# Optimization experiments

Hardware: AMD Instinct MI355X
Metric: run time of the kernel (lower is better)

## Reference

```python
import jax, jax.numpy as jnp
import numpy as np

B, P, E, A, M, D, V, L = 32, 196, 256, 512, 512, 512, 20000, 52


def setup_inputs() -> dict:
    key = jax.random.key(0)
    ks = jax.random.split(key, 16)
    u = lambda k, sh, s=0.05: (jax.random.normal(k, sh, jnp.float32) * s)
    lengths = jnp.sort(jax.random.randint(ks[2], (B,), 2, L + 1))[::-1].at[0].set(L)
    return dict(
        encoder_out=jax.random.normal(ks[0], (B, P, E), jnp.float32),
        encoded_captions=jax.random.randint(ks[1], (B, L), 0, V),
        caption_lengths=lengths,
        W_enc_att=u(ks[3], (E, A)), b_enc_att=jnp.zeros((A,), jnp.float32),
        W_dec_att=u(ks[4], (D, A)), b_dec_att=jnp.zeros((A,), jnp.float32),
        W_full_att=u(ks[5], (A, 1)), b_full_att=jnp.zeros((1,), jnp.float32),
        emb=u(ks[6], (V, M), 0.1),
        W_ih=u(ks[7], (M + E, 4 * D)), b_ih=jnp.zeros((4 * D,), jnp.float32),
        W_hh=u(ks[8], (D, 4 * D)), b_hh=jnp.zeros((4 * D,), jnp.float32),
        W_init_h=u(ks[9], (E, D)), b_init_h=jnp.zeros((D,), jnp.float32),
        W_init_c=u(ks[10], (E, D)), b_init_c=jnp.zeros((D,), jnp.float32),
        W_fbeta=u(ks[11], (D, E)), b_fbeta=jnp.zeros((E,), jnp.float32),
        W_fc=u(ks[12], (D, V), 0.1), b_fc=jnp.zeros((V,), jnp.float32),
    )


def reference(encoder_out, encoded_captions, caption_lengths,
              W_enc_att, b_enc_att, W_dec_att, b_dec_att, W_full_att, b_full_att,
              emb, W_ih, b_ih, W_hh, b_hh,
              W_init_h, b_init_h, W_init_c, b_init_c,
              W_fbeta, b_fbeta, W_fc, b_fc):
    # Dropout is identity in eval mode.
    T = encoded_captions.shape[1] - 1  # max decode length (max caption_length - 1)
    decode_lengths = caption_lengths - 1
    embs = emb[encoded_captions]                       # [B, L, M]
    mean_enc = encoder_out.mean(axis=1)                # [B, E]
    h0 = mean_enc @ W_init_h + b_init_h                # [B, D]
    c0 = mean_enc @ W_init_c + b_init_c
    att1 = encoder_out @ W_enc_att + b_enc_att         # [B, P, A], constant over time
    masks = (jnp.arange(T)[None, :] < decode_lengths[:, None]).T  # [T, B]
    emb_seq = jnp.swapaxes(embs[:, :T, :], 0, 1)       # [T, B, M]

    def step(carry, xs):
        h, c = carry
        e_t, m = xs                                    # [B, M], [B]
        att2 = h @ W_dec_att + b_dec_att               # [B, A]
        att = (jax.nn.relu(att1 + att2[:, None, :]) @ W_full_att)[..., 0] + b_full_att[0]  # [B, P]
        alpha = jax.nn.softmax(att, axis=1)            # [B, P]
        awe = jnp.einsum('bpe,bp->be', encoder_out, alpha)
        gate = jax.nn.sigmoid(h @ W_fbeta + b_fbeta)
        awe = gate * awe
        gates = jnp.concatenate([e_t, awe], axis=1) @ W_ih + b_ih + h @ W_hh + b_hh
        i, f, g, o = jnp.split(gates, 4, axis=1)       # torch LSTMCell gate order: i, f, g, o
        c_new = jax.nn.sigmoid(f) * c + jax.nn.sigmoid(i) * jnp.tanh(g)
        h_new = jax.nn.sigmoid(o) * jnp.tanh(c_new)
        preds = h_new @ W_fc + b_fc                    # [B, V]
        mm = m[:, None]
        # rows with l <= t are frozen (they were sliced away in the torch loop)
        h = jnp.where(mm, h_new, h)
        c = jnp.where(mm, c_new, c)
        preds = jnp.where(mm, preds, 0.0)
        alpha = jnp.where(mm, alpha, 0.0)
        return (h, c), (preds, alpha)

    (_, _), (preds, alphas) = jax.lax.scan(step, (h0, c0), (emb_seq, masks))
    predictions = jnp.swapaxes(preds, 0, 1)            # [B, T, V]
    alphas = jnp.swapaxes(alphas, 0, 1)                # [B, T, P]
    return predictions, encoded_captions, decode_lengths, alphas
```

## Files before the change

kernel.cpp:

```cpp
#include <hip/hip_runtime.h>
#include <hip/hip_bf16.h>
#include <math.h>
#include <stddef.h>


typedef unsigned short ushort_t;
typedef __bf16 bf16x8 __attribute__((ext_vector_type(8)));
typedef float f32x4 __attribute__((ext_vector_type(4)));
typedef unsigned short ushort8 __attribute__((ext_vector_type(8)));
typedef unsigned short ushort4v __attribute__((ext_vector_type(4)));
typedef unsigned long long u64_t;

union FragU { ushort8 u; bf16x8 b; };

__device__ __forceinline__ unsigned short f2bu(float f){
  union { float f; unsigned int i; } c; c.f = f;
  unsigned int x = c.i;
  unsigned int r = x + 0x7fffu + ((x >> 16) & 1u);
  return (unsigned short)(r >> 16);
}
__device__ __forceinline__ float bu2f(unsigned short u){
  union { unsigned int i; float f; } c; c.i = ((unsigned int)u) << 16; return c.f;
}
__device__ __forceinline__ float sigm(float x){ return 1.f/(1.f+__expf(-x)); }
__device__ __forceinline__ float ftanh(float x){ float e = __expf(2.f*x); return 1.f - 2.f/(e+1.f); }

__device__ __forceinline__ u64_t coh_ld64(const u64_t* p){
  return __hip_atomic_load(p, __ATOMIC_RELAXED, __HIP_MEMORY_SCOPE_AGENT);
}
__device__ __forceinline__ void coh_st64(u64_t* p, u64_t v){
  __hip_atomic_store(p, v, __ATOMIC_RELAXED, __HIP_MEMORY_SCOPE_AGENT);
}
__device__ __forceinline__ int coh_ldi(const int* p){
  return __hip_atomic_load(p, __ATOMIC_RELAXED, __HIP_MEMORY_SCOPE_AGENT);
}
__device__ __forceinline__ void coh_sti(int* p, int v){
  __hip_atomic_store(p, v, __ATOMIC_RELAXED, __HIP_MEMORY_SCOPE_AGENT);
}

#define FLG(f) ((f)*32)

__global__ __launch_bounds__(256) void k_cvtT(const float* __restrict__ src, int C,
                                              ushort_t* __restrict__ dst, int ldd, int perm){
  __shared__ float tile[32][33];
  int c0 = blockIdx.x*32, r0 = blockIdx.y*32;
  int tx = threadIdx.x & 31, ty = threadIdx.x >> 5;
  #pragma unroll
  for (int i=0;i<4;i++){ int r = ty + i*8; tile[r][tx] = src[(size_t)(r0+r)*C + c0+tx]; }
  __syncthreads();
  #pragma unroll
  for (int i=0;i<4;i++){
    int c = ty + i*8;
    int row = c0 + c;
    if (perm) row = ((row & 511) << 2) | (row >> 9);
    dst[(size_t)row*ldd + r0+tx] = f2bu(tile[tx][c]);
  }
}

__global__ __launch_bounds__(256) void k_cvt4(const float* __restrict__ src,
                                              ushort_t* __restrict__ dst, int n4){
  int i = blockIdx.x*256 + threadIdx.x;
  if (i < n4){
    float4 v = ((const float4*)src)[i];
    ushort4v o; o.x=f2bu(v.x); o.y=f2bu(v.y); o.z=f2bu(v.z); o.w=f2bu(v.w);
    ((ushort4v*)dst)[i] = o;
  }
}

__global__ __launch_bounds__(256) void k_misc(const int* __restrict__ cap, const int* __restrict__ lens,
                      const float* __restrict__ bdec, const float* __restrict__ bfb,
                      const float* __restrict__ bih, const float* __restrict__ bhh,
                      float* out_cap, float* out_dl, int* declen,
                      float* xbias, float* bihR, int* flags){
  int tid = blockIdx.x*256 + threadIdx.x;
  for (int i=tid; i<5120; i+=2048) flags[i] = 0;
  if (tid < 32*52) out_cap[tid] = (float)cap[tid];
  if (tid < 32){ int dl = lens[tid]-1; out_dl[tid] = (float)dl; declen[tid] = dl; }
  if (tid < 768) xbias[tid] = (tid<512) ? bdec[tid] : bfb[tid-512];
  if (tid < 2048){
    int c = (tid&3)*512 + (tid>>2);
    bihR[tid] = bih[c] + bhh[c];
  }
}

__global__ __launch_bounds__(256) void k_init(const float* __restrict__ enc,
                     const float* __restrict__ Wih_, const float* __restrict__ bih_,
                     const float* __restrict__ Wic_, const float* __restrict__ bic_,
                     ushort_t* __restrict__ hnewb, float* __restrict__ cbuf){
  int b = blockIdx.x, tid = threadIdx.x;
  __shared__ float mean_s[256];
  const float* eb = enc + (size_t)b*196*256;
  float s = 0.f;
  for (int p=0;p<196;p++) s += eb[p*256 + tid];
  mean_s[tid] = s * (1.f/196.f);
  __syncthreads();
  float h0=0.f,h1=0.f,c0=0.f,c1=0.f;
  for (int k=0;k<256;k++){
    float m = mean_s[k];
    h0 += m*Wih_[k*512+tid];      h1 += m*Wih_[k*512+tid+256];
    c0 += m*Wic_[k*512+tid];      c1 += m*Wic_[k*512+tid+256];
  }
  hnewb[b*512+tid]     = f2bu(h0 + bih_[tid]);
  hnewb[b*512+tid+256] = f2bu(h1 + bih_[tid+256]);
  cbuf[b*512+tid]      = c0 + bic_[tid];
  cbuf[b*512+tid+256]  = c1 + bic_[tid+256];
}

__global__ __launch_bounds__(256) void k_gather(const int* __restrict__ cap,
                                                const float* __restrict__ emb,
                                                ushort_t* __restrict__ erowsb){
  int row = blockIdx.x; int b = row/51, t = row%51;
  int tok = cap[b*52 + t];
  const float* src = emb + (size_t)tok*512;
  ushort_t* dst = erowsb + (size_t)row*512;
  dst[threadIdx.x]       = f2bu(src[threadIdx.x]);
  dst[threadIdx.x + 256] = f2bu(src[threadIdx.x + 256]);
}

#define LDT 40
__global__ __launch_bounds__(256)
void k_gemm(const ushort_t* __restrict__ Ag, int lda,
            const ushort_t* __restrict__ Bg, int ldb,
            int Mrows, int Ncols, int K,
            const float* __restrict__ bias,
            float* __restrict__ outF, ushort_t* __restrict__ outH, int ldo)
{
  __shared__ ushort_t As[128*LDT];
  __shared__ ushort_t Bs[128*LDT];
  int m0 = blockIdx.y*128, n0 = blockIdx.x*128;
  int tid = threadIdx.x;
  int wave = tid>>6, lane = tid&63;
  int wm = wave>>1, wn = wave&1;
  int q = lane>>4, r = lane&15;
  f32x4 acc[4][4];
  f32x4 zero4 = {0.f,0.f,0.f,0.f};
  #pragma unroll
  for(int i=0;i<4;i++){ acc[i][0]=zero4; acc[i][1]=zero4; acc[i][2]=zero4; acc[i][3]=zero4; }

  for (int k0=0; k0<K; k0+=32){
    __syncthreads();
    #pragma unroll
    for (int c=tid; c<512; c+=256){
      int row = c>>2, ko = (c&3)*8;
      ushort8 v = {0,0,0,0,0,0,0,0};
      if (m0+row < Mrows) v = *(const ushort8*)(Ag + (size_t)(m0+row)*lda + k0 + ko);
      *(ushort8*)(As + row*LDT + ko) = v;
      ushort8 wv = {0,0,0,0,0,0,0,0};
      if (n0+row < Ncols) wv = *(const ushort8*)(Bg + (size_t)(n0+row)*ldb + k0 + ko);
      *(ushort8*)(Bs + row*LDT + ko) = wv;
    }
    __syncthreads();
    FragU a[4], bb[4];
    #pragma unroll
    for(int i=0;i<4;i++){
      a[i].u  = *(const ushort8*)(As + (64*wm + 16*i + r)*LDT + 8*q);
      bb[i].u = *(const ushort8*)(Bs + (64*wn + 16*i + r)*LDT + 8*q);
    }
    #pragma unroll
    for(int i=0;i<4;i++)
      #pragma unroll
      for(int j=0;j<4;j++)
        acc[i][j] = __builtin_amdgcn_mfma_f32_16x16x32_bf16(a[i].b, bb[j].b, acc[i][j], 0,0,0);
  }
  #pragma unroll
  for(int i=0;i<4;i++){
    int rowbase = m0 + 64*wm + 16*i + q*4;
    #pragma unroll
    for(int j=0;j<4;j++){
      int col = n0 + 64*wn + 16*j + r;
      if (col >= Ncols) continue;
      float bv = bias ? bias[col] : 0.f;
      #pragma unroll
      for(int rr=0;rr<4;rr++){
        int row = rowbase + rr;
        if (row >= Mrows) continue;
        float v = acc[i][j][rr] + bv;
        if (outF) outF[(size_t)row*ldo + col] = v;
        else      outH[(size_t)row*ldo + col] = f2bu(v);
      }
    }
  }
}

__global__ __launch_bounds__(512)
void k_steps(const ushort_t* __restrict__ XWT768, const ushort_t* __restrict__ WHCp,
             const float* __restrict__ xbias,
             const ushort_t* __restrict__ att1b, const float* __restrict__ wfull,
             const ushort_t* __restrict__ encb, const ushort_t* __restrict__ eihR,
             const int* __restrict__ declen,
             ushort_t* __restrict__ hnewb, float* __restrict__ cbuf,
             float* __restrict__ XO,
             ushort_t* __restrict__ xaweb, ushort_t* __restrict__ hallb,
             float* __restrict__ out_alph,
             const ushort_t* __restrict__ WfcT, const float* __restrict__ bfc,
             float* __restrict__ out_preds, int* flags)
{
  __shared__ char pool[150272];
  int blk = blockIdx.x, tid = threadIdx.x;
  int wave = tid>>6, lane = tid&63;
  int q = lane>>4, r = lane&15;

  if (blk < 32){
    int b = blk, g = b>>4;
    float*    att2_s = (float*)pool;
    float*    wf_s   = (float*)(pool + 3072);
    float*    part_s = (float*)(pool + 5120);
    float*    awep_s = (float*)(pool + 6848);
    float*    alpha_s= (float*)(pool + 8896);
    float*    red_s  = (float*)(pool + 9728);
    ushort_t* xst    = (ushort_t*)(pool + 9856);
    if (tid < 512) wf_s[tid] = wfull[tid];
    __syncthreads();

    for (int t=0;t<51;t++){
      if (tid < 32) while (coh_ldi(flags + FLG(g*32 + tid)) < t+1) __builtin_amdgcn_s_sleep(1);
      __syncthreads();
      {
        const u64_t* src = (const u64_t*)(XO + (size_t)b*768);
        if (tid < 384) ((u64_t*)att2_s)[tid] = coh_ld64(src + tid);
      }
      __syncthreads();
      {
        int ph = tid>>8, p = tid&255;
        if (p < 196){
          const ushort_t* arow = att1b + ((size_t)b*196 + p)*512 + ph*256;
          const float* a2 = att2_s + ph*256;
          const float* wf = wf_s + ph*256;
          float s0=0.f,s1=0.f,s2=0.f,s3=0.f;
          for (int k=0;k<256;k+=8){
            ushort8 v = *(const ushort8*)(arow + k);
            s0 += fmaxf(bu2f(v[0]) + a2[k+0], 0.f)*wf[k+0];
            s1 += fmaxf(bu2f(v[1]) + a2[k+1], 0.f)*wf[k+1];
            s2 += fmaxf(bu2f(v[2]) + a2[k+2], 0.f)*wf[k+2];
            s3 += fmaxf(bu2f(v[3]) + a2[k+3], 0.f)*wf[k+3];
            s0 += fmaxf(bu2f(v[4]) + a2[k+4], 0.f)*wf[k+4];
            s1 += fmaxf(bu2f(v[5]) + a2[k+5], 0.f)*wf[k+5];
            s2 += fmaxf(bu2f(v[6]) + a2[k+6], 0.f)*wf[k+6];
            s3 += fmaxf(bu2f(v[7]) + a2[k+7], 0.f)*wf[k+7];
          }
          part_s[ph*208 + p] = (s0+s1)+(s2+s3);
        }
      }
      __syncthreads();
      float av = -1e30f;
      if (tid < 196) av = part_s[tid] + part_s[208 + tid];
      float m = av;
      #pragma unroll
      for (int off=32;off>0;off>>=1) m = fmaxf(m, __shfl_down(m, off, 64));
      if ((tid&63)==0) red_s[tid>>6] = m;
      __syncthreads();
      if (tid==0){
        float mm = red_s[0];
        #pragma unroll
        for (int i=1;i<8;i++) mm = fmaxf(mm, red_s[i]);
        red_s[16] = mm;
      }
      __syncthreads();
      float gmax = red_s[16];
      float ev = (tid<196) ? __expf(av - gmax) : 0.f;
      float ssum = ev;
      #pragma unroll
      for (int off=32;off>0;off>>=1) ssum += __shfl_down(ssum, off, 64);
      if ((tid&63)==0) red_s[20+(tid>>6)] = ssum;
      __syncthreads();
      if (tid==0){
        float s = 0.f;
        #pragma unroll
        for (int i=0;i<8;i++) s += red_s[20+i];
        red_s[17] = s;
      }
      __syncthreads();
      float inv = 1.f/red_s[17];
      int mask = (t < declen[b]) ? 1 : 0;
      if (tid<196){
        float al = ev*inv;
        alpha_s[tid] = al;
        out_alph[((size_t)b*51 + t)*196 + tid] = mask ? al : 0.f;
      }
      __syncthreads();
      {
        int e = tid&255, hh = tid>>8;
        const ushort_t* eb = encb + (size_t)b*196*256;
        float a0=0.f, a1=0.f;
        for (int pp=0;pp<98;pp+=2){
          int p0 = hh*98 + pp;
          a0 += alpha_s[p0]  *bu2f(eb[(size_t)p0*256 + e]);
          a1 += alpha_s[p0+1]*bu2f(eb[(size_t)(p0+1)*256 + e]);
        }
        awep_s[hh*256 + e] = a0+a1;
      }
      __syncthreads();
      if (tid < 256){
        float aw = awep_s[tid] + awep_s[256+tid];
        float gate = sigm(att2_s[512 + tid]);
        xst[tid] = f2bu(gate*aw);
      }
      __syncthreads();
      if (tid < 64){
        u64_t v = *(const u64_t*)(xst + tid*4);
        coh_st64((u64_t*)(xaweb + (size_t)b*256) + tid, v);
      }
      __syncthreads();
      if (tid==0) coh_sti(flags + FLG(128 + b), t+1);
    }
  } else if (blk < 96){
    int j = blk-32, g = j>>5, jj = j&31;
    int b0 = g*16;
    int n0b = jj*64;
    int n0x = jj*32;
    ushort_t* Wh = (ushort_t*)pool;
    ushort_t* Wc = (ushort_t*)(pool + 66560);
    ushort_t* Wx = (ushort_t*)(pool + 100352);
    ushort_t* As = (ushort_t*)(pool + 133632);
    float*    gl = (float*)(pool + 142080);
    ushort_t* hst= (ushort_t*)(pool + 146176);
    ushort_t* hstA=(ushort_t*)(pool + 146688);

    for (int i=tid; i<64*64; i+=512){ int row=i>>6, ko=(i&63)*8;
      *(ushort8*)(Wh + row*520 + ko) = *(const ushort8*)(WHCp + (size_t)(n0b+row)*768 + ko); }
    for (int i=tid; i<64*32; i+=512){ int row=i>>5, ko=(i&31)*8;
      *(ushort8*)(Wc + row*264 + ko) = *(const ushort8*)(WHCp + (size_t)(n0b+row)*768 + 512 + ko); }
    if (jj < 24)
      for (int i=tid; i<32*64; i+=512){ int row=i>>6, ko=(i&63)*8;
        *(ushort8*)(Wx + row*520 + ko) = *(const ushort8*)(XWT768 + (size_t)(n0x+row)*512 + ko); }
    __syncthreads();

    f32x4 gwh = {0.f,0.f,0.f,0.f};
    float hprev = 0.f;
    {
      const u64_t* H8 = (const u64_t*)(hnewb + (size_t)b0*512);
      for (int i=tid; i<2048; i+=512){ int row=i>>7, k4=i&127;
        *(u64_t*)(As + row*520 + k4*4) = coh_ld64(H8 + row*128 + k4); }
      __syncthreads();
      if (tid < 256) hprev = bu2f(As[(tid>>4)*520 + jj*16 + (tid&15)]);
      if (jj>=24 && tid==0) coh_sti(flags + FLG(g*32+jj), 1);
      if (jj<24 && wave<2){
        f32x4 xo = {0.f,0.f,0.f,0.f};
        for (int kc=0;kc<512;kc+=32){
          FragU a,bx;
          a.u  = *(const ushort8*)(As + r*520 + kc + 8*q);
          bx.u = *(const ushort8*)(Wx + (wave*16 + r)*520 + kc + 8*q);
          xo = __builtin_amdgcn_mfma_f32_16x16x32_bf16(bx.b, a.b, xo, 0,0,0);
        }
        int col0 = n0x + wave*16 + 4*q;
        float vv[4];
        #pragma unroll
        for (int rr=0;rr<4;rr++) vv[rr] = xo[rr] + xbias[col0+rr];
        u64_t* dst = (u64_t*)(XO + (size_t)(b0 + r)*768 + col0);
        coh_st64(dst+0, ((const u64_t*)vv)[0]);
        coh_st64(dst+1, ((const u64_t*)vv)[1]);
      }
      __syncthreads();
      if (jj<24 && tid==0) coh_sti(flags + FLG(g*32+jj), 1);
      if (wave < 4){
        for (int kc=0;kc<512;kc+=32){
          FragU a,bw;
          a.u  = *(const ushort8*)(As + r*520 + kc + 8*q);
          bw.u = *(const ushort8*)(Wh + (wave*16 + r)*520 + kc + 8*q);
          gwh = __builtin_amdgcn_mfma_f32_16x16x32_bf16(a.b, bw.b, gwh, 0,0,0);
        }
      }
    }

    for (int t=0;t<51;t++){
      float eih[4] = {0.f,0.f,0.f,0.f};
      if (wave < 4){
        #pragma unroll
        for (int rr=0;rr<4;rr++){
          int row = 4*q + rr;
          eih[rr] = bu2f(eihR[((size_t)(b0+row)*51 + t)*2048 + n0b + wave*16 + r]);
        }
      }
      if (tid < 16) while (coh_ldi(flags + FLG(128 + b0 + tid)) < t+1) __builtin_amdgcn_s_sleep(1);
      __syncthreads();
      const u64_t* X8 = (const u64_t*)(xaweb + (size_t)b0*256);
      for (int i=tid; i<1024; i+=512){ int row=i>>6, k4=i&63;
        *(u64_t*)(As + row*264 + k4*4) = coh_ld64(X8 + row*64 + k4); }
      __syncthreads();
      if (wave < 4){
        f32x4 cc = {0.f,0.f,0.f,0.f};
        for (int kc=0;kc<256;kc+=32){
          FragU a,bw;
          a.u  = *(const ushort8*)(As + r*264 + kc + 8*q);
          bw.u = *(const ushort8*)(Wc + (wave*16 + r)*264 + kc + 8*q);
          cc = __builtin_amdgcn_mfma_f32_16x16x32_bf16(a.b, bw.b, cc, 0,0,0);
        }
        #pragma unroll
        for (int rr=0;rr<4;rr++)
          gl[(4*q+rr)*64 + wave*16 + r] = gwh[rr] + cc[rr] + eih[rr];
      }
      __syncthreads();
      if (tid < 256){
        int bl = tid>>4, dd = tid&15;
        int bb = b0 + bl, d = jj*16 + dd;
        float gi = gl[bl*64 + dd*4+0], gf = gl[bl*64 + dd*4+1];
        float gg = gl[bl*64 + dd*4+2], go = gl[bl*64 + dd*4+3];
        float cold = cbuf[(size_t)bb*512 + d];
        float cnew = sigm(gf)*cold + sigm(gi)*ftanh(gg);
        float hnew = sigm(go)*ftanh(cnew);
        bool upd = (t < declen[bb]);
        if (upd) cbuf[(size_t)bb*512 + d] = cnew;
        float hkeep = upd ? hnew : hprev;
        hprev = hkeep;
        hst[tid]  = f2bu(hkeep);
        hstA[tid] = f2bu(hnew);
      }
      __syncthreads();
      if (tid < 64){
        int bl2 = tid>>2, o = tid&3;
        coh_st64((u64_t*)(hnewb + (size_t)(b0+bl2)*512 + jj*16) + o,
                 *(const u64_t*)(hst + tid*4));
        coh_st64((u64_t*)(hallb + ((size_t)((b0+bl2)*51 + t))*512 + jj*16) + o,
                 *(const u64_t*)(hstA + tid*4));
      }
      __syncthreads();
      if (tid==0) coh_sti(flags + FLG(64 + g*32 + jj), t+1);
      if (t == 50) break;

      if (tid < 32) while (coh_ldi(flags + FLG(64 + g*32 + tid)) < t+1) __builtin_amdgcn_s_sleep(1);
      __syncthreads();
      const u64_t* H8 = (const u64_t*)(hnewb + (size_t)b0*512);
      for (int i=tid; i<2048; i+=512){ int row=i>>7, k4=i&127;
        *(u64_t*)(As + row*520 + k4*4) = coh_ld64(H8 + row*128 + k4); }
      __syncthreads();
      if (jj>=24 && tid==0) coh_sti(flags + FLG(g*32+jj), t+2);
      if (jj<24 && wave<2){
        f32x4 xo = {0.f,0.f,0.f,0.f};
        for (int kc=0;kc<512;kc+=32){
          FragU a,bx;
          a.u  = *(const ushort8*)(As + r*520 + kc + 8*q);
          bx.u = *(const ushort8*)(Wx + (wave*16 + r)*520 + kc + 8*q);
          xo = __builtin_amdgcn_mfma_f32_16x16x32_bf16(bx.b, a.b, xo, 0,0,0);
        }
        int col0 = n0x + wave*16 + 4*q;
        float vv[4];
        #pragma unroll
        for (int rr=0;rr<4;rr++) vv[rr] = xo[rr] + xbias[col0+rr];
        u64_t* dst = (u64_t*)(XO + (size_t)(b0 + r)*768 + col0);
        coh_st64(dst+0, ((const u64_t*)vv)[0]);
        coh_st64(dst+1, ((const u64_t*)vv)[1]);
      }
      __syncthreads();
      if (jj<24 && tid==0) coh_sti(flags + FLG(g*32+jj), t+2);
      gwh = (f32x4){0.f,0.f,0.f,0.f};
      if (wave < 4){
        for (int kc=0;kc<512;kc+=32){
          FragU a,bw;
          a.u  = *(const ushort8*)(As + r*520 + kc + 8*q);
          bw.u = *(const ushort8*)(Wh + (wave*16 + r)*520 + kc + 8*q);
          gwh = __builtin_amdgcn_mfma_f32_16x16x32_bf16(a.b, bw.b, gwh, 0,0,0);
        }
      }
    }
  } else {
    int cs = blk - 96;
    int n0 = cs*128;
    ushort_t* As2 = (ushort_t*)pool;
    ushort_t* Bs2 = (ushort_t*)(pool + 66560);
    int til0 = wave*2, til1 = wave*2+1;
    int mt0 = til0>>3, nt0 = til0&7;
    int mt1 = til1>>3, nt1 = til1&7;

    for (int t=0;t<51;t++){
      if (tid < 64) while (coh_ldi(flags + FLG(64 + tid)) < t+1) __builtin_amdgcn_s_sleep(4);
      __syncthreads();
      for (int i=tid; i<4096; i+=512){
        int row = i>>7, k4 = i&127;
        *(u64_t*)(As2 + row*520 + k4*4) =
          coh_ld64((const u64_t*)hallb + (size_t)(row*51 + t)*128 + k4);
      }
      __syncthreads();
      f32x4 acc0 = {0.f,0.f,0.f,0.f}, acc1 = {0.f,0.f,0.f,0.f};
      for (int kc=0; kc<512; kc+=32){
        {
          int row = tid>>2, ko = (tid&3)*8;
          ushort8 wv = {0,0,0,0,0,0,0,0};
          int gr = n0 + row;
          if (gr < 20000) wv = *(const ushort8*)(WfcT + (size_t)gr*512 + kc + ko);
          *(ushort8*)(Bs2 + row*40 + ko) = wv;
        }
        __syncthreads();
        FragU a0,b0f,a1,b1f;
        a0.u  = *(const ushort8*)(As2 + (mt0*16 + r)*520 + kc + 8*q);
        b0f.u = *(const ushort8*)(Bs2 + (nt0*16 + r)*40 + 8*q);
        acc0 = __builtin_amdgcn_mfma_f32_16x16x32_bf16(a0.b, b0f.b, acc0, 0,0,0);
        a1.u  = *(const ushort8*)(As2 + (mt1*16 + r)*520 + kc + 8*q);
        b1f.u = *(const ushort8*)(Bs2 + (nt1*16 + r)*40 + 8*q);
        acc1 = __builtin_amdgcn_mfma_f32_16x16x32_bf16(a1.b, b1f.b, acc1, 0,0,0);
        __syncthreads();
      }
      {
        int colG = n0 + nt0*16 + r;
        if (colG < 20000){
          float bv = bfc[colG];
          #pragma unroll
          for (int rr=0;rr<4;rr++){
            int bidx = mt0*16 + 4*q + rr;
            float v = acc0[rr] + bv;
            if (t >= declen[bidx]) v = 0.f;
            out_preds[((size_t)(bidx*51 + t))*20000 + colG] = v;
          }
        }
      }
      {
        int colG = n0 + nt1*16 + r;
        if (colG < 20000){
          float bv = bfc[colG];
          #pragma unroll
          for (int rr=0;rr<4;rr++){
            int bidx = mt1*16 + 4*q + rr;
            float v = acc1[rr] + bv;
            if (t >= declen[bidx]) v = 0.f;
            out_preds[((size_t)(bidx*51 + t))*20000 + colG] = v;
          }
        }
      }
    }
  }
}

extern "C" void kernel_launch(void* const* d_in, const int* in_sizes, int n_in,
                              void* d_out, int out_size, void* d_ws, size_t ws_size,
                              hipStream_t stream)
{
  const float* enc   = (const float*)d_in[0];
  const int*   cap   = (const int*)d_in[1];
  const int*   lens  = (const int*)d_in[2];
  const float* Wenc  = (const float*)d_in[3];
  const float* benc  = (const float*)d_in[4];
  const float* Wdec  = (const float*)d_in[5];
  const float* bdec  = (const float*)d_in[6];
  const float* Wfull = (const float*)d_in[7];
  const float* emb   = (const float*)d_in[9];
  const float* Wih   = (const float*)d_in[10];
  const float* bih   = (const float*)d_in[11];
  const float* Whh   = (const float*)d_in[12];
  const float* bhh   = (const float*)d_in[13];
  const float* Winh  = (const float*)d_in[14];
  const float* binh  = (const float*)d_in[15];
  const float* Winc  = (const float*)d_in[16];
  const float* binc  = (const float*)d_in[17];
  const float* Wfb   = (const float*)d_in[18];
  const float* bfb   = (const float*)d_in[19];
  const float* Wfc   = (const float*)d_in[20];
  const float* bfc   = (const float*)d_in[21];
  float* out = (float*)d_out;

  char* w = (char*)d_ws;
  size_t off = 0;
  auto alloc = [&](size_t bytes)->char*{ char* p = w + off; off += (bytes + 255) & ~(size_t)255; return p; };
  ushort_t* WfcT    = (ushort_t*)alloc(20000ull*512*2);
  ushort_t* WHCp    = (ushort_t*)alloc(2048ull*768*2);
  ushort_t* WihTopTp= (ushort_t*)alloc(2048ull*512*2);
  ushort_t* XWT768  = (ushort_t*)alloc(768ull*512*2);
  ushort_t* WencT   = (ushort_t*)alloc(512ull*256*2);
  ushort_t* encb    = (ushort_t*)alloc(32ull*196*256*2);
  ushort_t* erowsb  = (ushort_t*)alloc(1632ull*512*2);
  ushort_t* att1b   = (ushort_t*)alloc(6272ull*512*2);
  ushort_t* eihR    = (ushort_t*)alloc(1632ull*2048*2);
  ushort_t* hallb   = (ushort_t*)alloc(1632ull*512*2);
  ushort_t* hnewb   = (ushort_t*)alloc(32ull*512*2);
  ushort_t* xaweb   = (ushort_t*)alloc(32ull*256*2);
  float*    XO      = (float*)alloc(32ull*768*4);
  float*    cbuf    = (float*)alloc(32ull*512*4);
  float*    xbias   = (float*)alloc(768*4);
  float*    bihR    = (float*)alloc(2048*4);
  int*      declen  = (int*)alloc(32*4);
  int*      flags   = (int*)alloc(20480);

  float* out_preds = out;
  float* out_cap   = out + 32640000ull;
  float* out_dl    = out_cap + 1664;
  float* out_alph  = out_dl + 32;

  k_cvtT<<<dim3(625,16),256,0,stream>>>(Wfc, 20000, WfcT, 512, 0);
  k_cvtT<<<dim3(64,16), 256,0,stream>>>(Whh, 2048, WHCp, 768, 1);
  k_cvtT<<<dim3(64,8),  256,0,stream>>>(Wih + 512ull*2048, 2048, WHCp + 512, 768, 1);
  k_cvtT<<<dim3(64,16), 256,0,stream>>>(Wih, 2048, WihTopTp, 512, 1);
  k_cvtT<<<dim3(16,16), 256,0,stream>>>(Wdec, 512, XWT768, 512, 0);
  k_cvtT<<<dim3(8,16),  256,0,stream>>>(Wfb, 256, XWT768 + 512ull*512, 512, 0);
  k_cvtT<<<dim3(16,8),  256,0,stream>>>(Wenc, 512, WencT, 256, 0);
  k_cvt4<<<1568,256,0,stream>>>(enc, encb, 401408);
  k_misc<<<8,256,0,stream>>>(cap, lens, bdec, bfb, bih, bhh, out_cap, out_dl, declen,
                             xbias, bihR, flags);
  k_init<<<32,256,0,stream>>>(enc, Winh, binh, Winc, binc, hnewb, cbuf);
  k_gather<<<1632,256,0,stream>>>(cap, emb, erowsb);
  k_gemm<<<dim3(4,49),256,0,stream>>>(encb, 256, WencT, 256, 6272, 512, 256,
                                      benc, nullptr, att1b, 512);
  k_gemm<<<dim3(16,13),256,0,stream>>>(erowsb, 512, WihTopTp, 512, 1632, 2048, 512,
                                       bihR, nullptr, eihR, 2048);

  k_steps<<<253,512,0,stream>>>(XWT768, WHCp, xbias, att1b, Wfull, encb, eihR, declen,
                                hnewb, cbuf, XO, xaweb, hallb, out_alph,
                                WfcT, bfc, out_preds, flags);
}
```

Before: 1.165 ms.

## Fuse preprocessing kernels and move Wfc conversion into idle persistent FC blocks

Merges the many small preprocessing launches (transposes, enc conversion, misc setup, init state, embedding gather) into one multi-role kernel to cut launch overhead. The large W_fc transpose/bf16 conversion moves into the FC blocks of the persistent step kernel, so it can overlap with the recurrent blocks' first steps instead of running ahead serially. It also trims softmax reductions by having every thread reduce the per-wave partials directly, and defers the alpha output store until after the flag signal. The in-kernel Wfc conversion reads columns with a strided, uncoalesced pattern, which may be slow.

```diff
diff --git a/kernel.cpp b/kernel.cpp
--- a/kernel.cpp
+++ b/kernel.cpp
@@ -40,81 +40,93 @@
 
 #define FLG(f) ((f)*32)
 
-__global__ __launch_bounds__(256) void k_cvtT(const float* __restrict__ src, int C,
-                                              ushort_t* __restrict__ dst, int ldd, int perm){
-  __shared__ float tile[32][33];
-  int c0 = blockIdx.x*32, r0 = blockIdx.y*32;
-  int tx = threadIdx.x & 31, ty = threadIdx.x >> 5;
+__device__ __forceinline__ void d_cvtT(const float* __restrict__ src, int C,
+                                       ushort_t* __restrict__ dst, int ldd, int perm,
+                                       int bx, int by, int tid, float* tile ){
+  int c0 = bx*32, r0 = by*32;
+  int tx = tid & 31, ty = tid >> 5;
   #pragma unroll
-  for (int i=0;i<4;i++){ int r = ty + i*8; tile[r][tx] = src[(size_t)(r0+r)*C + c0+tx]; }
+  for (int i=0;i<4;i++){ int r = ty + i*8; tile[r*33+tx] = src[(size_t)(r0+r)*C + c0+tx]; }
   __syncthreads();
   #pragma unroll
   for (int i=0;i<4;i++){
     int c = ty + i*8;
     int row = c0 + c;
     if (perm) row = ((row & 511) << 2) | (row >> 9);
-    dst[(size_t)row*ldd + r0+tx] = f2bu(tile[tx][c]);
-  }
-}
-
-__global__ __launch_bounds__(256) void k_cvt4(const float* __restrict__ src,
-                                              ushort_t* __restrict__ dst, int n4){
-  int i = blockIdx.x*256 + threadIdx.x;
-  if (i < n4){
-    float4 v = ((const float4*)src)[i];
-    ushort4v o; o.x=f2bu(v.x); o.y=f2bu(v.y); o.z=f2bu(v.z); o.w=f2bu(v.w);
-    ((ushort4v*)dst)[i] = o;
-  }
-}
-
-__global__ __launch_bounds__(256) void k_misc(const int* __restrict__ cap, const int* __restrict__ lens,
-                      const float* __restrict__ bdec, const float* __restrict__ bfb,
-                      const float* __restrict__ bih, const float* __restrict__ bhh,
-                      float* out_cap, float* out_dl, int* declen,
-                      float* xbias, float* bihR, int* flags){
-  int tid = blockIdx.x*256 + threadIdx.x;
-  for (int i=tid; i<5120; i+=2048) flags[i] = 0;
-  if (tid < 32*52) out_cap[tid] = (float)cap[tid];
-  if (tid < 32){ int dl = lens[tid]-1; out_dl[tid] = (float)dl; declen[tid] = dl; }
-  if (tid < 768) xbias[tid] = (tid<512) ? bdec[tid] : bfb[tid-512];
-  if (tid < 2048){
-    int c = (tid&3)*512 + (tid>>2);
-    bihR[tid] = bih[c] + bhh[c];
-  }
-}
-
-__global__ __launch_bounds__(256) void k_init(const float* __restrict__ enc,
-                     const float* __restrict__ Wih_, const float* __restrict__ bih_,
-                     const float* __restrict__ Wic_, const float* __restrict__ bic_,
-                     ushort_t* __restrict__ hnewb, float* __restrict__ cbuf){
-  int b = blockIdx.x, tid = threadIdx.x;
-  __shared__ float mean_s[256];
-  const float* eb = enc + (size_t)b*196*256;
-  float s = 0.f;
-  for (int p=0;p<196;p++) s += eb[p*256 + tid];
-  mean_s[tid] = s * (1.f/196.f);
-  __syncthreads();
-  float h0=0.f,h1=0.f,c0=0.f,c1=0.f;
-  for (int k=0;k<256;k++){
-    float m = mean_s[k];
-    h0 += m*Wih_[k*512+tid];      h1 += m*Wih_[k*512+tid+256];
-    c0 += m*Wic_[k*512+tid];      c1 += m*Wic_[k*512+tid+256];
-  }
-  hnewb[b*512+tid]     = f2bu(h0 + bih_[tid]);
-  hnewb[b*512+tid+256] = f2bu(h1 + bih_[tid+256]);
-  cbuf[b*512+tid]      = c0 + bic_[tid];
-  cbuf[b*512+tid+256]  = c1 + bic_[tid+256];
-}
-
-__global__ __launch_bounds__(256) void k_gather(const int* __restrict__ cap,
-                                                const float* __restrict__ emb,
-                                                ushort_t* __restrict__ erowsb){
-  int row = blockIdx.x; int b = row/51, t = row%51;
-  int tok = cap[b*52 + t];
-  const float* src = emb + (size_t)tok*512;
-  ushort_t* dst = erowsb + (size_t)row*512;
-  dst[threadIdx.x]       = f2bu(src[threadIdx.x]);
-  dst[threadIdx.x + 256] = f2bu(src[threadIdx.x + 256]);
+    dst[(size_t)row*ldd + r0+tx] = f2bu(tile[tx*33+c]);
+  }
+}
+
+__global__ __launch_bounds__(256)
+void k_pre1(const float* __restrict__ Whh, const float* __restrict__ Wih,
+            const float* __restrict__ Wdec, const float* __restrict__ Wfb,
+            const float* __restrict__ Wenc, const float* __restrict__ enc,
+            const int* __restrict__ cap, const int* __restrict__ lens,
+            const float* __restrict__ bdec, const float* __restrict__ bfb,
+            const float* __restrict__ bih, const float* __restrict__ bhh,
+            const float* __restrict__ Winh, const float* __restrict__ binh,
+            const float* __restrict__ Winc, const float* __restrict__ binc,
+            const float* __restrict__ emb,
+            ushort_t* WHCp, ushort_t* WihTopTp, ushort_t* XWT768, ushort_t* WencT,
+            ushort_t* encb, float* out_cap, float* out_dl, int* declen,
+            float* xbias, float* bihR, int* flags,
+            ushort_t* hnewb, float* cbuf, ushort_t* erowsb)
+{
+  __shared__ float smem_f[1056];
+  int blk = blockIdx.x, tid = threadIdx.x;
+  if (blk < 1024){        d_cvtT(Whh, 2048, WHCp, 768, 1, blk&63, blk>>6, tid, smem_f); }
+  else if (blk < 1536){   int i=blk-1024; d_cvtT(Wih + 512ull*2048, 2048, WHCp+512, 768, 1, i&63, i>>6, tid, smem_f); }
+  else if (blk < 2560){   int i=blk-1536; d_cvtT(Wih, 2048, WihTopTp, 512, 1, i&63, i>>6, tid, smem_f); }
+  else if (blk < 2816){   int i=blk-2560; d_cvtT(Wdec, 512, XWT768, 512, 0, i&15, i>>4, tid, smem_f); }
+  else if (blk < 2944){   int i=blk-2816; d_cvtT(Wfb, 256, XWT768 + 512ull*512, 512, 0, i&7, i>>3, tid, smem_f); }
+  else if (blk < 3072){   int i=blk-2944; d_cvtT(Wenc, 512, WencT, 256, 0, i&15, i>>4, tid, smem_f); }
+  else if (blk < 4640){
+    int i = (blk-3072)*256 + tid;
+    if (i < 401408){
+      float4 v = ((const float4*)enc)[i];
+      ushort4v o; o.x=f2bu(v.x); o.y=f2bu(v.y); o.z=f2bu(v.z); o.w=f2bu(v.w);
+      ((ushort4v*)encb)[i] = o;
+    }
+  }
+  else if (blk < 4648){
+    int gtid = (blk-4640)*256 + tid;
+    for (int i=gtid; i<5120; i+=2048) flags[i] = 0;
+    if (gtid < 32*52) out_cap[gtid] = (float)cap[gtid];
+    if (gtid < 32){ int dl = lens[gtid]-1; out_dl[gtid] = (float)dl; declen[gtid] = dl; }
+    if (gtid < 768) xbias[gtid] = (gtid<512) ? bdec[gtid] : bfb[gtid-512];
+    if (gtid < 2048){
+      int c = (gtid&3)*512 + (gtid>>2);
+      bihR[gtid] = bih[c] + bhh[c];
+    }
+  }
+  else if (blk < 4680){
+    int b = blk-4648;
+    float* mean_s = smem_f;
+    const float* eb = enc + (size_t)b*196*256;
+    float s = 0.f;
+    for (int p=0;p<196;p++) s += eb[p*256 + tid];
+    mean_s[tid] = s * (1.f/196.f);
+    __syncthreads();
+    float h0=0.f,h1=0.f,c0=0.f,c1=0.f;
+    for (int k=0;k<256;k++){
+      float m = mean_s[k];
+      h0 += m*Winh[k*512+tid];      h1 += m*Winh[k*512+tid+256];
+      c0 += m*Winc[k*512+tid];      c1 += m*Winc[k*512+tid+256];
+    }
+    hnewb[b*512+tid]     = f2bu(h0 + binh[tid]);
+    hnewb[b*512+tid+256] = f2bu(h1 + binh[tid+256]);
+    cbuf[b*512+tid]      = c0 + binc[tid];
+    cbuf[b*512+tid+256]  = c1 + binc[tid+256];
+  }
+  else {
+    int row = blk-4680;
+    int b = row/51, t = row%51;
+    int tok = cap[b*52 + t];
+    const float* src = emb + (size_t)tok*512;
+    ushort_t* dst = erowsb + (size_t)row*512;
+    dst[tid]       = f2bu(src[tid]);
+    dst[tid + 256] = f2bu(src[tid + 256]);
+  }
 }
 
 #define LDT 40
@@ -192,7 +204,8 @@
              float* __restrict__ XO,
              ushort_t* __restrict__ xaweb, ushort_t* __restrict__ hallb,
              float* __restrict__ out_alph,
-             const ushort_t* __restrict__ WfcT, const float* __restrict__ bfc,
+             const float* __restrict__ Wfc, ushort_t* __restrict__ WfcT,
+             const float* __restrict__ bfc,
              float* __restrict__ out_preds, int* flags)
 {
   __shared__ char pool[150272];
@@ -249,34 +262,21 @@
       for (int off=32;off>0;off>>=1) m = fmaxf(m, __shfl_down(m, off, 64));
       if ((tid&63)==0) red_s[tid>>6] = m;
       __syncthreads();
-      if (tid==0){
-        float mm = red_s[0];
-        #pragma unroll
-        for (int i=1;i<8;i++) mm = fmaxf(mm, red_s[i]);
-        red_s[16] = mm;
-      }
-      __syncthreads();
-      float gmax = red_s[16];
+      float gmax = red_s[0];
+      #pragma unroll
+      for (int i=1;i<8;i++) gmax = fmaxf(gmax, red_s[i]);
       float ev = (tid<196) ? __expf(av - gmax) : 0.f;
       float ssum = ev;
       #pragma unroll
       for (int off=32;off>0;off>>=1) ssum += __shfl_down(ssum, off, 64);
-      if ((tid&63)==0) red_s[20+(tid>>6)] = ssum;
-      __syncthreads();
-      if (tid==0){
-        float s = 0.f;
-        #pragma unroll
-        for (int i=0;i<8;i++) s += red_s[20+i];
-        red_s[17] = s;
-      }
-      __syncthreads();
-      float inv = 1.f/red_s[17];
-      int mask = (t < declen[b]) ? 1 : 0;
-      if (tid<196){
-        float al = ev*inv;
-        alpha_s[tid] = al;
-        out_alph[((size_t)b*51 + t)*196 + tid] = mask ? al : 0.f;
-      }
+      if ((tid&63)==0) red_s[8+(tid>>6)] = ssum;
+      __syncthreads();
+      float stot = red_s[8];
+      #pragma unroll
+      for (int i=9;i<16;i++) stot += red_s[i];
+      float inv = 1.f/stot;
+      float al = (tid<196) ? ev*inv : 0.f;
+      if (tid<196) alpha_s[tid] = al;
       __syncthreads();
       {
         int e = tid&255, hh = tid>>8;
@@ -302,6 +302,10 @@
       }
       __syncthreads();
       if (tid==0) coh_sti(flags + FLG(128 + b), t+1);
+      if (tid<196){
+        int mask = (t < declen[b]) ? 1 : 0;
+        out_alph[((size_t)b*51 + t)*196 + tid] = mask ? al : 0.f;
+      }
     }
   } else if (blk < 96){
     int j = blk-32, g = j>>5, jj = j&31;
@@ -460,6 +464,25 @@
     int til0 = wave*2, til1 = wave*2+1;
     int mt0 = til0>>3, nt0 = til0&7;
     int mt1 = til1>>3, nt1 = til1&7;
+
+    {
+      ushort_t* cvt = (ushort_t*)pool;
+      int jc = tid & 127, kq = tid >> 7;
+      int gcol = n0 + jc;
+      if (gcol < 20000){
+        for (int kk=0; kk<128; kk++){
+          int k = kq*128 + kk;
+          cvt[jc*520 + k] = f2bu(Wfc[(size_t)k*20000 + gcol]);
+        }
+      }
+      __syncthreads();
+      for (int i=tid; i<128*64; i+=512){
+        int row = i>>6, ko = (i&63)*8;
+        if (n0+row < 20000)
+          *(ushort8*)(WfcT + (size_t)(n0+row)*512 + ko) = *(const ushort8*)(cvt + row*520 + ko);
+      }
+      __syncthreads();
+    }
 
     for (int t=0;t<51;t++){
       if (tid < 64) while (coh_ldi(flags + FLG(64 + tid)) < t+1) __builtin_amdgcn_s_sleep(4);
@@ -573,18 +596,11 @@
   float* out_dl    = out_cap + 1664;
   float* out_alph  = out_dl + 32;
 
-  k_cvtT<<<dim3(625,16),256,0,stream>>>(Wfc, 20000, WfcT, 512, 0);
-  k_cvtT<<<dim3(64,16), 256,0,stream>>>(Whh, 2048, WHCp, 768, 1);
-  k_cvtT<<<dim3(64,8),  256,0,stream>>>(Wih + 512ull*2048, 2048, WHCp + 512, 768, 1);
-  k_cvtT<<<dim3(64,16), 256,0,stream>>>(Wih, 2048, WihTopTp, 512, 1);
-  k_cvtT<<<dim3(16,16), 256,0,stream>>>(Wdec, 512, XWT768, 512, 0);
-  k_cvtT<<<dim3(8,16),  256,0,stream>>>(Wfb, 256, XWT768 + 512ull*512, 512, 0);
-  k_cvtT<<<dim3(16,8),  256,0,stream>>>(Wenc, 512, WencT, 256, 0);
-  k_cvt4<<<1568,256,0,stream>>>(enc, encb, 401408);
-  k_misc<<<8,256,0,stream>>>(cap, lens, bdec, bfb, bih, bhh, out_cap, out_dl, declen,
-                             xbias, bihR, flags);
-  k_init<<<32,256,0,stream>>>(enc, Winh, binh, Winc, binc, hnewb, cbuf);
-  k_gather<<<1632,256,0,stream>>>(cap, emb, erowsb);
+  k_pre1<<<6312,256,0,stream>>>(Whh, Wih, Wdec, Wfb, Wenc, enc, cap, lens,
+                                bdec, bfb, bih, bhh, Winh, binh, Winc, binc, emb,
+                                WHCp, WihTopTp, XWT768, WencT, encb,
+                                out_cap, out_dl, declen, xbias, bihR, flags,
+                                hnewb, cbuf, erowsb);
   k_gemm<<<dim3(4,49),256,0,stream>>>(encb, 256, WencT, 256, 6272, 512, 256,
                                       benc, nullptr, att1b, 512);
   k_gemm<<<dim3(16,13),256,0,stream>>>(erowsb, 512, WihTopTp, 512, 1632, 2048, 512,
@@ -592,5 +608,5 @@
 
   k_steps<<<253,512,0,stream>>>(XWT768, WHCp, xbias, att1b, Wfull, encb, eihR, declen,
                                 hnewb, cbuf, XO, xaweb, hallb, out_alph,
-                                WfcT, bfc, out_preds, flags);
-}
+                                Wfc, WfcT, bfc, out_preds, flags);
+}
```

New measurement: 1.116 ms. 1.04x faster.
